# Performance work log

Measured on AMD Instinct MI355X. Metric: run time of the kernel, lower is better.

The kernel has to match this reference:

```python
import jax, jax.numpy as jnp
import numpy as np

K, N, M, P, H = 8, 16, 8, 32, 32
BSZ, T = 128, 512
TAU = 0.5
P_STAY = 0.9


def setup_inputs() -> dict:
    key = jax.random.key(0)
    ks = jax.random.split(key, 20)
    f32 = jnp.float32
    norm = lambda k, s, sc=1.0: (jax.random.normal(k, s) * sc).astype(f32)
    sw = 1.0 / np.sqrt(H)  # torch GRU init scale
    return {
        "a_seq": norm(ks[0], (BSZ, T, P)),
        "A": norm(ks[1], (K, N, N), 0.1),
        "Bmat": norm(ks[2], (K, N, M), 0.1),
        "C": norm(ks[3], (K, P, N), 0.1),
        "Q": (jnp.tile(jnp.eye(N, dtype=f32)[None], (K, 1, 1)) + norm(ks[4], (K, N, N), 0.01)),
        "wih_f": norm(ks[5], (3 * H, P), sw),
        "whh_f": norm(ks[6], (3 * H, H), sw),
        "bih_f": norm(ks[7], (3 * H,), sw),
        "bhh_f": norm(ks[8], (3 * H,), sw),
        "wih_b": norm(ks[9], (3 * H, P), sw),
        "whh_b": norm(ks[10], (3 * H, H), sw),
        "bih_b": norm(ks[11], (3 * H,), sw),
        "bhh_b": norm(ks[12], (3 * H,), sw),
        "wl": norm(ks[13], (K * K, 2 * H), sw),
        "bl": norm(ks[14], (K * K,), sw),
        "wi": norm(ks[15], (K, 2 * H), sw),
        "bi": norm(ks[16], (K,), sw),
        "u0": jax.random.uniform(ks[17], (BSZ, K), minval=1e-6, maxval=1.0 - 1e-6, dtype=f32),
        "useq": jax.random.uniform(ks[18], (BSZ, T - 1, K), minval=1e-6, maxval=1.0 - 1e-6, dtype=f32),
    }


def _gru_dir(gx, whh, bhh, reverse):
    # gx: [T, B, 3H] precomputed input-to-hidden gates; torch GRU cell math
    def step(h, g):
        gh = h @ whh.T + bhh
        xr, xz, xn = jnp.split(g, 3, axis=-1)
        hr, hz, hn = jnp.split(gh, 3, axis=-1)
        r = jax.nn.sigmoid(xr + hr)
        z = jax.nn.sigmoid(xz + hz)
        n = jnp.tanh(xn + r * hn)
        h_new = (1.0 - z) * n + z * h
        return h_new, h_new
    h0 = jnp.zeros((gx.shape[1], whh.shape[1]), gx.dtype)
    _, hs = jax.lax.scan(step, h0, gx, reverse=reverse)
    return hs  # [T, B, H]


def reference(a_seq, A, Bmat, C, Q, wih_f, whh_f, bih_f, bhh_f,
              wih_b, whh_b, bih_b, bhh_b, wl, bl, wi, bi, u0, useq):
    Bn, Tn, _ = a_seq.shape
    Kn = A.shape[0]
    x = a_seq.transpose(1, 0, 2)  # [T, B, P]
    hf = _gru_dir(x @ wih_f.T + bih_f, whh_f, bhh_f, False)
    hb = _gru_dir(x @ wih_b.T + bih_b, whh_b, bhh_b, True)
    h_seq = jnp.concatenate([hf, hb], axis=-1)  # [T, B, 2H]

    logits = (h_seq @ wl.T + bl).reshape(Tn, Bn, Kn, Kn)  # [T, B, K, K]
    init_logits = h_seq[0] @ wi.T + bi                     # [B, K]

    g0 = -jnp.log(-jnp.log(u0))
    gseq = -jnp.log(-jnp.log(useq))  # [B, T-1, K]

    # t = 0 (soft gumbel-softmax since is_training=True)
    y0 = jax.nn.softmax((init_logits + g0) / TAU, axis=-1)
    lq0 = (y0 * jax.nn.log_softmax(init_logits, axis=-1)).sum(-1)
    lp0 = (y0 * jnp.log(1.0 / Kn)).sum(-1)  # torch: full_like(1/K).log()

    trans = jnp.full((Kn, Kn), (1.0 - P_STAY) / (Kn - 1), a_seq.dtype)
    trans = trans.at[jnp.arange(Kn), jnp.arange(Kn)].set(P_STAY)

    def step(y_prev, xs):
        lg, g = xs  # lg: [B, K, K], g: [B, K]
        l_t = jnp.einsum('bk,bkj->bj', y_prev, lg)
        y_t = jax.nn.softmax((l_t + g) / TAU, axis=-1)
        lq = (y_t * jax.nn.log_softmax(l_t, axis=-1)).sum(-1)
        tp = y_prev @ trans
        lp = (y_t * jnp.log(jnp.clip(tp, 1e-8))).sum(-1)
        return y_t, (y_t, lq, lp)

    _, (ys, lqs, lps) = jax.lax.scan(step, y0, (logits[1:], gseq.transpose(1, 0, 2)))

    y_seq = jnp.concatenate([y0[None], ys], axis=0).transpose(1, 0, 2)  # [B, T, K]
    log_qseq = jnp.concatenate([lq0[None], lqs], axis=0).T              # [B, T]
    log_pseq = jnp.concatenate([lp0[None], lps], axis=0).T              # [B, T]

    A_seq = jnp.einsum('btk,kij->btij', y_seq, A)
    B_seq = jnp.einsum('btk,knm->btnm', y_seq, Bmat)
    Q_seq = jnp.einsum('btk,kij->btij', y_seq, Q)
    C_seq = jnp.broadcast_to(C[0], (Bn, Tn) + C[0].shape)
    return (A_seq, B_seq, C_seq, Q_seq, log_qseq, log_pseq)
```

## Files before the change

### kernel.cpp

```cpp
#include <hip/hip_runtime.h>
#include <math.h>

#define T 512
#define B 128
#define KK 8
#define HH 32
#define PP 32

#define WS_GX    0
#define WS_HSEQ  12582912
#define WS_LOGITS 0
#define WS_INIT  16777216
#define WS_YSEQ  16778240

#define OUT_A    0
#define OUT_B    16777216
#define OUT_C    25165824
#define OUT_Q    58720256
#define OUT_LQ   75497472
#define OUT_LP   75563008

#define TINV 2.0f
#define PSTAY 0.9f
#define OFFV (0.1f / 7.0f)
#define DPS (PSTAY - OFFV)
#define LOG_INV_K (-2.0794415416798357f)

typedef float f4v __attribute__((ext_vector_type(4)));
typedef __attribute__((address_space(3))) float as3f;

__device__ __forceinline__ void dma16(unsigned ldsbyte, int voffbyte, const void* sbase) {
    asm volatile("s_mov_b32 m0, %0\n\t"
                 "global_load_lds_dwordx4 %1, %2"
                 :: "s"(ldsbyte), "v"(voffbyte), "s"(sbase)
                 : "memory");
}
__device__ __forceinline__ void st16(void* p, f4v v) {
    asm volatile("global_store_dwordx4 %0, %1, off" :: "v"(p), "v"(v) : "memory");
}
__device__ __forceinline__ f4v ldsr16(int addr) {
    f4v out;
    asm volatile("ds_read_b128 %0, %1" : "=v"(out) : "v"(addr));
    return out;
}
__device__ __forceinline__ f4v ldg16(const void* p) {
    f4v out;
    asm volatile("global_load_dwordx4 %0, %1, off" : "=v"(out) : "v"(p) : "memory");
    return out;
}
__device__ __forceinline__ float ldg4(const void* p) {
    float out;
    asm volatile("global_load_dword %0, %1, off" : "=v"(out) : "v"(p) : "memory");
    return out;
}

__global__ __launch_bounds__(192) void gx_kernel(
    const float* __restrict__ a_seq,
    const float* __restrict__ wih_f, const float* __restrict__ bih_f,
    const float* __restrict__ wih_b, const float* __restrict__ bih_b,
    float* __restrict__ gx,
    const float* __restrict__ u0, const float* __restrict__ useq,
    float* __restrict__ gs) {
    __shared__ float xt[64 * 32];
    if (blockIdx.x >= 1024) {
        int id = (blockIdx.x - 1024) * 192 + threadIdx.x;
        if (id < T * B * KK) {
            int j = id & 7;
            int b = (id >> 3) & 127;
            int t = id >> 10;
            float u = (t == 0) ? u0[b * 8 + j]
                               : useq[((size_t)b * (T - 1) + (t - 1)) * 8 + j];
            gs[id] = -logf(-logf(u)) * TINV;
        }
        return;
    }
    int blk = blockIdx.x;
    int b = blk >> 3;
    int t0 = (blk & 7) << 6;
    int g = threadIdx.x;
    int dir = (g >= 96) ? 1 : 0;
    int gg = dir ? (g - 96) : g;
    const float* w = dir ? wih_b : wih_f;
    const float* bv = dir ? bih_b : bih_f;

    {
        const float4* src = (const float4*)(a_seq + ((size_t)b * T + t0) * PP);
        float4* dst = (float4*)xt;
        for (int idx = g; idx < 512; idx += 192) dst[idx] = src[idx];
    }
    float wreg[32];
#pragma unroll
    for (int q = 0; q < 8; ++q) {
        float4 wv = *(const float4*)(w + (size_t)gg * PP + q * 4);
        wreg[q * 4 + 0] = wv.x; wreg[q * 4 + 1] = wv.y;
        wreg[q * 4 + 2] = wv.z; wreg[q * 4 + 3] = wv.w;
    }
    float bias = bv[gg];
    __syncthreads();

    float* op = gx + ((size_t)(dir * B + b) * T + t0) * 96 + gg;
#pragma unroll 4
    for (int r = 0; r < 64; ++r) {
        const float4* xr = (const float4*)(xt + r * 32);
        float acc = bias;
#pragma unroll
        for (int q = 0; q < 8; ++q) {
            float4 xv = xr[q];
            acc = fmaf(xv.x, wreg[q * 4 + 0], acc);
            acc = fmaf(xv.y, wreg[q * 4 + 1], acc);
            acc = fmaf(xv.z, wreg[q * 4 + 2], acc);
            acc = fmaf(xv.w, wreg[q * 4 + 3], acc);
        }
        op[(size_t)r * 96] = acc;
    }
}

__global__ __launch_bounds__(64, 1) void gru_kernel(
    const float* __restrict__ gx,
    const float* __restrict__ whh_f, const float* __restrict__ bhh_f,
    const float* __restrict__ whh_b, const float* __restrict__ bhh_b,
    float* __restrict__ hseq) {
    int cid = blockIdx.x;
    int b = cid & 127;
    int dir = cid >> 7;
    int i = threadIdx.x & 31;
    const float* whh = dir ? whh_b : whh_f;
    const float* bhh = dir ? bhh_b : bhh_f;
    const float* gp0 = gx + (size_t)cid * (T * 96);

    f4v wr[8], wz[8], wn[8];
#pragma unroll
    for (int q = 0; q < 8; ++q) {
        wr[q] = ldg16(whh + (size_t)i * 32 + q * 4);
        wz[q] = ldg16(whh + (size_t)(32 + i) * 32 + q * 4);
        wn[q] = ldg16(whh + (size_t)(64 + i) * 32 + q * 4);
    }
    float bhr = ldg4(bhh + i);
    float bhz = ldg4(bhh + 32 + i);
    float bhn = ldg4(bhh + 64 + i);

    const float* p = gp0 + (dir ? (T - 1) * 96 : 0);
    int gstep = dir ? -96 : 96;
    int voff = (((dir ? (T - 1) : 0) * B + b) * 64 + dir * 32 + i) * 4;
    int vstep = dir ? -(B * 64 * 4) : (B * 64 * 4);

    float pxrA[8], pxzA[8], pxnA[8], pxrB[8], pxzB[8], pxnB[8];

#define LOADG(PR, PZ, PN, G0) do {                                             \
        _Pragma("unroll")                                                      \
        for (int u_ = 0; u_ < 8; ++u_) {                                       \
            int sc_ = (G0) * 8 + u_; if (sc_ > T - 1) sc_ = T - 1;             \
            const float* rp_ = p + sc_ * gstep;                                \
            PR[u_] = ldg4(rp_ + i);                                            \
            PZ[u_] = ldg4(rp_ + 32 + i);                                       \
            PN[u_] = ldg4(rp_ + 64 + i);                                       \
        }                                                                      \
    } while (0)

#define GWAIT(N) do {                                                          \
        asm volatile("s_waitcnt vmcnt(" #N ")" ::: "memory");                  \
        __builtin_amdgcn_sched_barrier(0);                                     \
    } while (0)

#define GSTEP(PR, PZ, PN, SLOT) do {                                           \
        float hj_[32];                                                         \
        _Pragma("unroll")                                                      \
        for (int jj = 0; jj < 32; ++jj)                                        \
            hj_[jj] = __uint_as_float(                                         \
                __builtin_amdgcn_readlane(__float_as_uint(h), jj));            \
        __builtin_amdgcn_sched_barrier(0);                                     \
        float r0_ = PR[SLOT] + bhr, r1_ = 0.f, r2_ = 0.f, r3_ = 0.f;           \
        float z0_ = PZ[SLOT] + bhz, z1_ = 0.f, z2_ = 0.f, z3_ = 0.f;           \
        float n0_ = bhn, n1_ = 0.f, n2_ = 0.f, n3_ = 0.f;                      \
        _Pragma("unroll")                                                      \
        for (int q_ = 0; q_ < 2; ++q_) {                                       \
            _Pragma("unroll")                                                  \
            for (int c_ = 0; c_ < 4; ++c_) {                                   \
                float hv_ = hj_[q_ * 4 + c_];                                  \
                r0_ = fmaf(wr[q_][c_], hv_, r0_);                              \
                z0_ = fmaf(wz[q_][c_], hv_, z0_);                              \
                n0_ = fmaf(wn[q_][c_], hv_, n0_);                              \
            }                                                                  \
        }                                                                      \
        _Pragma("unroll")                                                      \
        for (int q_ = 2; q_ < 4; ++q_) {                                       \
            _Pragma("unroll")                                                  \
            for (int c_ = 0; c_ < 4; ++c_) {                                   \
                float hv_ = hj_[q_ * 4 + c_];                                  \
                r1_ = fmaf(wr[q_][c_], hv_, r1_);                              \
                z1_ = fmaf(wz[q_][c_], hv_, z1_);                              \
                n1_ = fmaf(wn[q_][c_], hv_, n1_);                              \
            }                                                                  \
        }                                                                      \
        _Pragma("unroll")                                                      \
        for (int q_ = 4; q_ < 6; ++q_) {                                       \
            _Pragma("unroll")                                                  \
            for (int c_ = 0; c_ < 4; ++c_) {                                   \
                float hv_ = hj_[q_ * 4 + c_];                                  \
                r2_ = fmaf(wr[q_][c_], hv_, r2_);                              \
                z2_ = fmaf(wz[q_][c_], hv_, z2_);                              \
                n2_ = fmaf(wn[q_][c_], hv_, n2_);                              \
            }                                                                  \
        }                                                                      \
        _Pragma("unroll")                                                      \
        for (int q_ = 6; q_ < 8; ++q_) {                                       \
            _Pragma("unroll")                                                  \
            for (int c_ = 0; c_ < 4; ++c_) {                                   \
                float hv_ = hj_[q_ * 4 + c_];                                  \
                r3_ = fmaf(wr[q_][c_], hv_, r3_);                              \
                z3_ = fmaf(wz[q_][c_], hv_, z3_);                              \
                n3_ = fmaf(wn[q_][c_], hv_, n3_);                              \
            }                                                                  \
        }                                                                      \
        float hr_ = (r0_ + r1_) + (r2_ + r3_);                                 \
        float hz_ = (z0_ + z1_) + (z2_ + z3_);                                 \
        float hn_ = (n0_ + n1_) + (n2_ + n3_);                                 \
        float r_ = __builtin_amdgcn_rcpf(1.f + __expf(-hr_));                  \
        float z_ = __builtin_amdgcn_rcpf(1.f + __expf(-hz_));                  \
        float na_ = fmaf(r_, hn_, PN[SLOT]);                                   \
        float e2_ = __expf(-2.f * fabsf(na_));                                 \
        float n_ = copysignf((1.f - e2_) * __builtin_amdgcn_rcpf(1.f + e2_), na_); \
        h = fmaf(z_, h - n_, n_);                                              \
        asm volatile("global_store_dword %0, %1, %2"                           \
                     :: "v"(voff), "v"(h), "s"(hseq) : "memory");              \
        voff += vstep;                                                         \
    } while (0)

    LOADG(pxrA, pxzA, pxnA, 0);
    GWAIT(0);
    float h = 0.f;

    for (int gq = 0; gq < 32; ++gq) {
        LOADG(pxrB, pxzB, pxnB, 2 * gq + 1);
        GWAIT(32);
        GSTEP(pxrA, pxzA, pxnA, 0); GSTEP(pxrA, pxzA, pxnA, 1);
        GSTEP(pxrA, pxzA, pxnA, 2); GSTEP(pxrA, pxzA, pxnA, 3);
        GSTEP(pxrA, pxzA, pxnA, 4); GSTEP(pxrA, pxzA, pxnA, 5);
        GSTEP(pxrA, pxzA, pxnA, 6); GSTEP(pxrA, pxzA, pxnA, 7);
        LOADG(pxrA, pxzA, pxnA, 2 * gq + 2);
        GWAIT(32);
        GSTEP(pxrB, pxzB, pxnB, 0); GSTEP(pxrB, pxzB, pxnB, 1);
        GSTEP(pxrB, pxzB, pxnB, 2); GSTEP(pxrB, pxzB, pxnB, 3);
        GSTEP(pxrB, pxzB, pxnB, 4); GSTEP(pxrB, pxzB, pxnB, 5);
        GSTEP(pxrB, pxzB, pxnB, 6); GSTEP(pxrB, pxzB, pxnB, 7);
    }
#undef LOADG
#undef GWAIT
#undef GSTEP
}

__global__ __launch_bounds__(256) void logits_kernel(
    const float* __restrict__ hseq,
    const float* __restrict__ wl, const float* __restrict__ bl,
    const float* __restrict__ wi, const float* __restrict__ bi,
    float* __restrict__ logits, float* __restrict__ initl) {
    __shared__ float wls[64 * 65];
    __shared__ float hrow[4][64];
    int tid = threadIdx.x;
    for (int i2 = tid; i2 < 1024; i2 += 256) {
        float4 v = ((const float4*)wl)[i2];
        int gr = i2 >> 4;
        int cc = (i2 & 15) * 4;
        float* d = &wls[gr * 65 + cc];
        d[0] = v.x; d[1] = v.y; d[2] = v.z; d[3] = v.w;
    }
    int q = tid >> 6;
    int tb = blockIdx.x * 4 + q;
    int g = tid & 63;
    hrow[q][g] = hseq[(size_t)tb * 64 + g];
    __syncthreads();
    float acc = bl[g];
    const float* wrow = &wls[g * 65];
#pragma unroll
    for (int c = 0; c < 64; ++c) acc = fmaf(wrow[c], hrow[q][c], acc);
    logits[(size_t)tb * 64 + g] = acc * TINV;
    if (tb < B && g < 8) {
        float a2 = bi[g];
        const float* w2 = wi + (size_t)g * 64;
#pragma unroll
        for (int c = 0; c < 64; ++c) a2 = fmaf(w2[c], hrow[q][c], a2);
        initl[tb * 8 + g] = a2;
    }
}

__global__ __launch_bounds__(128, 1) void scan_kernel(
    const float* __restrict__ logits, const float* __restrict__ initl,
    const float* __restrict__ gs, float* __restrict__ yseq) {
    __shared__ float lds[6][2304];
    int tid = threadIdx.x;
    int wave = tid >> 6;
    int r = tid & 63;
    int b0 = blockIdx.x * 32;
    int b = b0 + (r & 31);
    int k15 = r & 15;

    unsigned ldsU = (unsigned)(unsigned long long)(as3f*)(&lds[0][0]);

#define ISSUE(tt, sl) do {                                                   \
        unsigned lb_ = ldsU + (unsigned)((sl) * 9216);                       \
        const char* bt_ = (const char*)logits + (size_t)(tt) * 32768;        \
        const char* gt_ = (const char*)gs + (size_t)(tt) * 4096;             \
        dma16(lb_ + 0 * 1024u, lof[0], bt_);                                 \
        dma16(lb_ + 1 * 1024u, lof[1], bt_);                                 \
        dma16(lb_ + 2 * 1024u, lof[2], bt_);                                 \
        dma16(lb_ + 3 * 1024u, lof[3], bt_);                                 \
        dma16(lb_ + 4 * 1024u, lof[4], bt_);                                 \
        dma16(lb_ + 5 * 1024u, lof[5], bt_);                                 \
        dma16(lb_ + 6 * 1024u, lof[6], bt_);                                 \
        dma16(lb_ + 7 * 1024u, lof[7], bt_);                                 \
        dma16(lb_ + 8192u, gof, gt_);                                        \
    } while (0)

    if (wave == 1) {
        int lof[8];
#pragma unroll
        for (int q = 0; q < 8; ++q) {
            int rr = q * 4 + (r >> 4);
            int cc = r & 15;
            lof[q] = (((b0 + rr) * 64) + ((cc ^ (rr & 15)) << 2)) << 2;
        }
        int gof;
        {
            int rg = r >> 1;
            int cc = r & 1;
            gof = (((b0 + rg) * 8) + ((cc ^ (rg & 1)) << 2)) << 2;
        }
#pragma unroll
        for (int p = 1; p <= 5; ++p) ISSUE(p, p);
        asm volatile("s_waitcnt vmcnt(36)" ::: "memory");
        __builtin_amdgcn_s_barrier();
        for (int t = 1; t < T; ++t) {
            asm volatile("s_waitcnt vmcnt(27)" ::: "memory");
            __builtin_amdgcn_s_barrier();
            int tp = t + 5; if (tp > T - 1) tp = T - 1;
            ISSUE(tp, (t + 5) % 6);
        }
        return;
    }

    unsigned rbase = ldsU + (unsigned)((r & 31) * 256);
    unsigned gbase = ldsU + 8192u + (unsigned)((r & 31) * 32);

#define SREAD(LL, GA, GB, tt) do {                                           \
        int so_ = ((tt) % 6) * 9216;                                         \
        _Pragma("unroll")                                                    \
        for (int m_ = 0; m_ < 16; ++m_)                                      \
            LL[m_] = ldsr16((int)(rbase + so_ + ((m_ ^ k15) << 4)));         \
        GA = ldsr16((int)(gbase + so_ + ((r & 1) << 4)));                    \
        GB = ldsr16((int)(gbase + so_ + (((r & 1) ^ 1) << 4)));              \
    } while (0)

#define LWAIT() do {                                                         \
        asm volatile("s_waitcnt lgkmcnt(0)" ::: "memory");                   \
        __builtin_amdgcn_sched_barrier(0);                                   \
    } while (0)

#define SCOMP(LL, GA, GB, tt) do {                                           \
        float pl_[8];                                                        \
        _Pragma("unroll")                                                    \
        for (int j_ = 0; j_ < 8; ++j_) pl_[j_] = 0.f;                        \
        _Pragma("unroll")                                                    \
        for (int k_ = 0; k_ < 8; ++k_) {                                     \
            f4v w0_ = LL[2 * k_], w1_ = LL[2 * k_ + 1];                      \
            float ek_ = e[k_];                                               \
            pl_[0] = fmaf(ek_, w0_.x, pl_[0]); pl_[1] = fmaf(ek_, w0_.y, pl_[1]); \
            pl_[2] = fmaf(ek_, w0_.z, pl_[2]); pl_[3] = fmaf(ek_, w0_.w, pl_[3]); \
            pl_[4] = fmaf(ek_, w1_.x, pl_[4]); pl_[5] = fmaf(ek_, w1_.y, pl_[5]); \
            pl_[6] = fmaf(ek_, w1_.z, pl_[6]); pl_[7] = fmaf(ek_, w1_.w, pl_[7]); \
        }                                                                    \
        float gg_[8] = {GA.x, GA.y, GA.z, GA.w, GB.x, GB.y, GB.z, GB.w};     \
        float ss_ = 0.f;                                                     \
        _Pragma("unroll")                                                    \
        for (int j_ = 0; j_ < 8; ++j_) {                                     \
            float a_ = fmaf(pl_[j_], sinv, gg_[j_]);                         \
            e[j_] = __expf(a_);                                              \
            ss_ += e[j_];                                                    \
        }                                                                    \
        sinv = __builtin_amdgcn_rcpf(ss_);                                   \
        if (r < 32) {                                                        \
            f4v v0_ = (f4v){e[0] * sinv, e[1] * sinv, e[2] * sinv, e[3] * sinv}; \
            f4v v1_ = (f4v){e[4] * sinv, e[5] * sinv, e[6] * sinv, e[7] * sinv}; \
            st16(&yp[2 * (tt)], v0_);                                        \
            st16(&yp[2 * (tt) + 1], v1_);                                    \
        }                                                                    \
    } while (0)

    f4v* yp = (f4v*)(yseq + (size_t)b * T * 8);
    float e[8];
    float sinv;

    {
        const f4v* il4 = (const f4v*)(initl + b * 8);
        f4v i0 = il4[0], i1 = il4[1];
        const f4v* g4 = (const f4v*)(gs + b * 8);
        f4v G0 = g4[0], G1 = g4[1];
        float a[8];
        a[0] = fmaf(i0.x, TINV, G0.x); a[1] = fmaf(i0.y, TINV, G0.y);
        a[2] = fmaf(i0.z, TINV, G0.z); a[3] = fmaf(i0.w, TINV, G0.w);
        a[4] = fmaf(i1.x, TINV, G1.x); a[5] = fmaf(i1.y, TINV, G1.y);
        a[6] = fmaf(i1.z, TINV, G1.z); a[7] = fmaf(i1.w, TINV, G1.w);
        float ssum = 0.f;
#pragma unroll
        for (int j = 0; j < 8; ++j) { e[j] = __expf(a[j]); ssum += e[j]; }
        sinv = __builtin_amdgcn_rcpf(ssum);
        if (r < 32) {
            f4v y0v = (f4v){e[0] * sinv, e[1] * sinv, e[2] * sinv, e[3] * sinv};
            f4v y1v = (f4v){e[4] * sinv, e[5] * sinv, e[6] * sinv, e[7] * sinv};
            st16(&yp[0], y0v);
            st16(&yp[1], y1v);
        }
    }

    f4v LA[16], LB[16], gaA, gbA, gaB, gbB;

    __builtin_amdgcn_s_barrier();
    SREAD(LA, gaA, gbA, 1);

    for (int t = 1; t < T - 1; t += 2) {
        __builtin_amdgcn_s_barrier();
        LWAIT();
        SREAD(LB, gaB, gbB, t + 1);
        SCOMP(LA, gaA, gbA, t);

        __builtin_amdgcn_s_barrier();
        LWAIT();
        SREAD(LA, gaA, gbA, t + 2);
        SCOMP(LB, gaB, gbB, t + 1);
    }
    __builtin_amdgcn_s_barrier();
    LWAIT();
    SCOMP(LA, gaA, gbA, T - 1);
#undef ISSUE
#undef SREAD
#undef LWAIT
#undef SCOMP
}

__global__ __launch_bounds__(256) void lqlp_kernel(
    const float* __restrict__ logits, const float* __restrict__ initl,
    const float* __restrict__ yseq,
    float* __restrict__ logq, float* __restrict__ logp) {
    int tid = blockIdx.x * 256 + threadIdx.x;
    int j = tid & 7;
    int row = tid >> 3;
    int b = row >> 9;
    int t = row & (T - 1);

    const float4* yt4 = (const float4*)(yseq + (size_t)row * 8);
    float4 ya = yt4[0], yb = yt4[1];
    float yt[8] = {ya.x, ya.y, ya.z, ya.w, yb.x, yb.y, yb.z, yb.w};

    float l[8];
    float lp;
    if (t == 0) {
        const float4* il4 = (const float4*)(initl + b * 8);
        float4 i0 = il4[0], i1 = il4[1];
        l[0] = i0.x; l[1] = i0.y; l[2] = i0.z; l[3] = i0.w;
        l[4] = i1.x; l[5] = i1.y; l[6] = i1.z; l[7] = i1.w;
        float sy = ((yt[0] + yt[1]) + (yt[2] + yt[3])) + ((yt[4] + yt[5]) + (yt[6] + yt[7]));
        lp = LOG_INV_K * sy;
    } else {
        const float4* yp4 = (const float4*)(yseq + (size_t)row * 8 - 8);
        float4 p0 = yp4[0], p1 = yp4[1];
        float ypv[8] = {p0.x, p0.y, p0.z, p0.w, p1.x, p1.y, p1.z, p1.w};
        float ypj = yseq[(size_t)row * 8 - 8 + j];
        const float4* L4 = (const float4*)(logits + ((size_t)t * B + b) * 64 + j * 8);
        float4 r0 = L4[0], r1 = L4[1];
        float c[8] = {ypj * r0.x, ypj * r0.y, ypj * r0.z, ypj * r0.w,
                      ypj * r1.x, ypj * r1.y, ypj * r1.z, ypj * r1.w};
#pragma unroll
        for (int s = 1; s <= 4; s <<= 1) {
#pragma unroll
            for (int m = 0; m < 8; ++m) c[m] += __shfl_xor(c[m], s, 64);
        }
#pragma unroll
        for (int m = 0; m < 8; ++m) l[m] = c[m] * 0.5f;
        float sy = ((ypv[0] + ypv[1]) + (ypv[2] + ypv[3])) + ((ypv[4] + ypv[5]) + (ypv[6] + ypv[7]));
        float acc = 0.f;
#pragma unroll
        for (int m = 0; m < 8; ++m) {
            float tp = fmaf(DPS, ypv[m], OFFV * sy);
            acc = fmaf(yt[m], logf(fmaxf(tp, 1e-8f)), acc);
        }
        lp = acc;
    }
    float m = fmaxf(fmaxf(fmaxf(l[0], l[1]), fmaxf(l[2], l[3])),
                    fmaxf(fmaxf(l[4], l[5]), fmaxf(l[6], l[7])));
    float se = 0.f;
#pragma unroll
    for (int m2 = 0; m2 < 8; ++m2) se += __expf(l[m2] - m);
    float lse = m + logf(se);
    float lq = 0.f;
#pragma unroll
    for (int m2 = 0; m2 < 8; ++m2) lq = fmaf(yt[m2], l[m2] - lse, lq);
    if (j == 0) {
        logq[row] = lq;
        logp[row] = lp;
    }
}

__global__ __launch_bounds__(256) void out_kernel(
    const float* __restrict__ yseq,
    const float* __restrict__ A, const float* __restrict__ Bm,
    const float* __restrict__ C, const float* __restrict__ Q,
    float4* __restrict__ out4) {
    __shared__ float tab[6144];
    int tid = threadIdx.x;
    int bt0 = blockIdx.x * 64;
    {
        float4* t4 = (float4*)tab;
        const float4* A4 = (const float4*)A;
        const float4* B4 = (const float4*)Bm;
        const float4* Q4 = (const float4*)Q;
        const float4* C4 = (const float4*)C;
        for (int i2 = tid; i2 < 512; i2 += 256) t4[i2] = A4[i2];
        if (tid < 256) t4[512 + tid] = B4[tid];
        for (int i2 = tid; i2 < 512; i2 += 256) t4[768 + i2] = Q4[i2];
        if (tid < 128) t4[1280 + tid] = C4[tid];
        const float4* Y4 = (const float4*)(yseq + (size_t)bt0 * 8);
        if (tid < 128) t4[1408 + tid] = Y4[tid];
    }
    __syncthreads();

    int wave = tid >> 6;
    int lane = tid & 63;
    const float4* t4 = (const float4*)tab;

    if (wave == 0 || wave == 1) {
        int tbase = (wave == 0) ? 0 : 768;
        size_t obase = (wave == 0) ? (size_t)(OUT_A / 4) : (size_t)(OUT_Q / 4);
        float4 wreg[8];
#pragma unroll
        for (int k = 0; k < 8; ++k) wreg[k] = t4[tbase + k * 64 + lane];
        for (int bt = 0; bt < 64; ++bt) {
            float4 ya = t4[1408 + bt * 2];
            float4 yb = t4[1408 + bt * 2 + 1];
            float yk[8] = {ya.x, ya.y, ya.z, ya.w, yb.x, yb.y, yb.z, yb.w};
            float4 v = make_float4(0.f, 0.f, 0.f, 0.f);
#pragma unroll
            for (int k = 0; k < 8; ++k) {
                v.x = fmaf(yk[k], wreg[k].x, v.x);
                v.y = fmaf(yk[k], wreg[k].y, v.y);
                v.z = fmaf(yk[k], wreg[k].z, v.z);
                v.w = fmaf(yk[k], wreg[k].w, v.w);
            }
            out4[obase + (size_t)(bt0 + bt) * 64 + lane] = v;
        }
    } else if (wave == 2) {
        if (lane < 32) {
            float4 wreg[8];
#pragma unroll
            for (int k = 0; k < 8; ++k) wreg[k] = t4[512 + k * 32 + lane];
            for (int bt = 0; bt < 64; ++bt) {
                float4 ya = t4[1408 + bt * 2];
                float4 yb = t4[1408 + bt * 2 + 1];
                float yk[8] = {ya.x, ya.y, ya.z, ya.w, yb.x, yb.y, yb.z, yb.w};
                float4 v = make_float4(0.f, 0.f, 0.f, 0.f);
#pragma unroll
                for (int k = 0; k < 8; ++k) {
                    v.x = fmaf(yk[k], wreg[k].x, v.x);
                    v.y = fmaf(yk[k], wreg[k].y, v.y);
                    v.z = fmaf(yk[k], wreg[k].z, v.z);
                    v.w = fmaf(yk[k], wreg[k].w, v.w);
                }
                out4[(size_t)(OUT_B / 4) + (size_t)(bt0 + bt) * 32 + lane] = v;
            }
        } else {
            float4 c0 = t4[1280 + (lane - 32)];
            for (int bt = 0; bt < 64; ++bt)
                out4[(size_t)(OUT_C / 4) + (size_t)(bt0 + bt) * 128 + (lane - 32)] = c0;
        }
    } else {
        float4 c1 = t4[1280 + 32 + lane];
        float4 c2 = (lane < 32) ? t4[1280 + 96 + lane] : make_float4(0.f, 0.f, 0.f, 0.f);
        for (int bt = 0; bt < 64; ++bt) {
            out4[(size_t)(OUT_C / 4) + (size_t)(bt0 + bt) * 128 + 32 + lane] = c1;
            if (lane < 32)
                out4[(size_t)(OUT_C / 4) + (size_t)(bt0 + bt) * 128 + 96 + lane] = c2;
        }
    }
}

extern "C" void kernel_launch(void* const* d_in, const int* in_sizes, int n_in,
                              void* d_out, int out_size, void* d_ws, size_t ws_size,
                              hipStream_t stream) {
    const float* a_seq = (const float*)d_in[0];
    const float* A     = (const float*)d_in[1];
    const float* Bmat  = (const float*)d_in[2];
    const float* C     = (const float*)d_in[3];
    const float* Q     = (const float*)d_in[4];
    const float* wih_f = (const float*)d_in[5];
    const float* whh_f = (const float*)d_in[6];
    const float* bih_f = (const float*)d_in[7];
    const float* bhh_f = (const float*)d_in[8];
    const float* wih_b = (const float*)d_in[9];
    const float* whh_b = (const float*)d_in[10];
    const float* bih_b = (const float*)d_in[11];
    const float* bhh_b = (const float*)d_in[12];
    const float* wl    = (const float*)d_in[13];
    const float* bl    = (const float*)d_in[14];
    const float* wi    = (const float*)d_in[15];
    const float* bi    = (const float*)d_in[16];
    const float* u0    = (const float*)d_in[17];
    const float* useq  = (const float*)d_in[18];

    float* ws = (float*)d_ws;
    float* gx     = ws + WS_GX;
    float* hseq   = ws + WS_HSEQ;
    float* logits = ws + WS_LOGITS;
    float* initl  = ws + WS_INIT;
    float* yseq   = ws + WS_YSEQ;
    float* gs2    = ws + WS_YSEQ + (size_t)B * T * KK;

    float* outf = (float*)d_out;
    float* logq = outf + OUT_LQ;
    float* logp = outf + OUT_LP;

    gx_kernel<<<1024 + (T * B * KK + 191) / 192, 192, 0, stream>>>(
        a_seq, wih_f, bih_f, wih_b, bih_b, gx, u0, useq, gs2);
    gru_kernel<<<256, 64, 0, stream>>>(gx, whh_f, bhh_f, whh_b, bhh_b, hseq);
    logits_kernel<<<T * B / 4, 256, 0, stream>>>(hseq, wl, bl, wi, bi, logits, initl);
    scan_kernel<<<4, 128, 0, stream>>>(logits, initl, gs2, yseq);
    lqlp_kernel<<<B * T * KK / 256, 256, 0, stream>>>(logits, initl, yseq, logq, logp);
    out_kernel<<<B * T / 64, 256, 0, stream>>>(yseq, A, Bmat, C, Q, (float4*)d_out);
}
```

Measured before the change: 454.5 us.

## Overlap C broadcast writes with the serial scan using extra scan blocks

```diff
diff --git a/kernel.cpp b/kernel.cpp
--- a/kernel.cpp
+++ b/kernel.cpp
@@ -285,9 +285,18 @@
 
 __global__ __launch_bounds__(128, 1) void scan_kernel(
     const float* __restrict__ logits, const float* __restrict__ initl,
-    const float* __restrict__ gs, float* __restrict__ yseq) {
+    const float* __restrict__ gs, float* __restrict__ yseq,
+    const float4* __restrict__ Csrc, float4* __restrict__ outC) {
     __shared__ float lds[6][2304];
     int tid = threadIdx.x;
+    if (blockIdx.x >= 4) {
+        size_t stride = (size_t)(2048 - 4) * 128;
+        for (size_t idx = (size_t)(blockIdx.x - 4) * 128 + tid;
+             idx < (size_t)B * T * 128; idx += stride) {
+            outC[idx] = Csrc[idx & 127];
+        }
+        return;
+    }
     int wave = tid >> 6;
     int r = tid & 63;
     int b0 = blockIdx.x * 32;
@@ -502,9 +511,9 @@
 __global__ __launch_bounds__(256) void out_kernel(
     const float* __restrict__ yseq,
     const float* __restrict__ A, const float* __restrict__ Bm,
-    const float* __restrict__ C, const float* __restrict__ Q,
+    const float* __restrict__ Q,
     float4* __restrict__ out4) {
-    __shared__ float tab[6144];
+    __shared__ float tab[5632];
     int tid = threadIdx.x;
     int bt0 = blockIdx.x * 64;
     {
@@ -512,13 +521,11 @@
         const float4* A4 = (const float4*)A;
         const float4* B4 = (const float4*)Bm;
         const float4* Q4 = (const float4*)Q;
-        const float4* C4 = (const float4*)C;
         for (int i2 = tid; i2 < 512; i2 += 256) t4[i2] = A4[i2];
         if (tid < 256) t4[512 + tid] = B4[tid];
         for (int i2 = tid; i2 < 512; i2 += 256) t4[768 + i2] = Q4[i2];
-        if (tid < 128) t4[1280 + tid] = C4[tid];
         const float4* Y4 = (const float4*)(yseq + (size_t)bt0 * 8);
-        if (tid < 128) t4[1408 + tid] = Y4[tid];
+        if (tid < 128) t4[1280 + tid] = Y4[tid];
     }
     __syncthreads();
 
@@ -533,8 +540,8 @@
 #pragma unroll
         for (int k = 0; k < 8; ++k) wreg[k] = t4[tbase + k * 64 + lane];
         for (int bt = 0; bt < 64; ++bt) {
-            float4 ya = t4[1408 + bt * 2];
-            float4 yb = t4[1408 + bt * 2 + 1];
+            float4 ya = t4[1280 + bt * 2];
+            float4 yb = t4[1280 + bt * 2 + 1];
             float yk[8] = {ya.x, ya.y, ya.z, ya.w, yb.x, yb.y, yb.z, yb.w};
             float4 v = make_float4(0.f, 0.f, 0.f, 0.f);
 #pragma unroll
@@ -546,37 +553,23 @@
             }
             out4[obase + (size_t)(bt0 + bt) * 64 + lane] = v;
         }
-    } else if (wave == 2) {
-        if (lane < 32) {
-            float4 wreg[8];
-#pragma unroll
-            for (int k = 0; k < 8; ++k) wreg[k] = t4[512 + k * 32 + lane];
-            for (int bt = 0; bt < 64; ++bt) {
-                float4 ya = t4[1408 + bt * 2];
-                float4 yb = t4[1408 + bt * 2 + 1];
-                float yk[8] = {ya.x, ya.y, ya.z, ya.w, yb.x, yb.y, yb.z, yb.w};
-                float4 v = make_float4(0.f, 0.f, 0.f, 0.f);
-#pragma unroll
-                for (int k = 0; k < 8; ++k) {
-                    v.x = fmaf(yk[k], wreg[k].x, v.x);
-                    v.y = fmaf(yk[k], wreg[k].y, v.y);
-                    v.z = fmaf(yk[k], wreg[k].z, v.z);
-                    v.w = fmaf(yk[k], wreg[k].w, v.w);
-                }
-                out4[(size_t)(OUT_B / 4) + (size_t)(bt0 + bt) * 32 + lane] = v;
+    } else if (wave == 2 && lane < 32) {
+        float4 wreg[8];
+#pragma unroll
+        for (int k = 0; k < 8; ++k) wreg[k] = t4[512 + k * 32 + lane];
+        for (int bt = 0; bt < 64; ++bt) {
+            float4 ya = t4[1280 + bt * 2];
+            float4 yb = t4[1280 + bt * 2 + 1];
+            float yk[8] = {ya.x, ya.y, ya.z, ya.w, yb.x, yb.y, yb.z, yb.w};
+            float4 v = make_float4(0.f, 0.f, 0.f, 0.f);
+#pragma unroll
+            for (int k = 0; k < 8; ++k) {
+                v.x = fmaf(yk[k], wreg[k].x, v.x);
+                v.y = fmaf(yk[k], wreg[k].y, v.y);
+                v.z = fmaf(yk[k], wreg[k].z, v.z);
+                v.w = fmaf(yk[k], wreg[k].w, v.w);
             }
-        } else {
-            float4 c0 = t4[1280 + (lane - 32)];
-            for (int bt = 0; bt < 64; ++bt)
-                out4[(size_t)(OUT_C / 4) + (size_t)(bt0 + bt) * 128 + (lane - 32)] = c0;
-        }
-    } else {
-        float4 c1 = t4[1280 + 32 + lane];
-        float4 c2 = (lane < 32) ? t4[1280 + 96 + lane] : make_float4(0.f, 0.f, 0.f, 0.f);
-        for (int bt = 0; bt < 64; ++bt) {
-            out4[(size_t)(OUT_C / 4) + (size_t)(bt0 + bt) * 128 + 32 + lane] = c1;
-            if (lane < 32)
-                out4[(size_t)(OUT_C / 4) + (size_t)(bt0 + bt) * 128 + 96 + lane] = c2;
+            out4[(size_t)(OUT_B / 4) + (size_t)(bt0 + bt) * 32 + lane] = v;
         }
     }
 }
@@ -615,12 +608,14 @@
     float* outf = (float*)d_out;
     float* logq = outf + OUT_LQ;
     float* logp = outf + OUT_LP;
+    float4* outC = (float4*)(outf + OUT_C);
 
     gx_kernel<<<1024 + (T * B * KK + 191) / 192, 192, 0, stream>>>(
         a_seq, wih_f, bih_f, wih_b, bih_b, gx, u0, useq, gs2);
     gru_kernel<<<256, 64, 0, stream>>>(gx, whh_f, bhh_f, whh_b, bhh_b, hseq);
     logits_kernel<<<T * B / 4, 256, 0, stream>>>(hseq, wl, bl, wi, bi, logits, initl);
-    scan_kernel<<<4, 128, 0, stream>>>(logits, initl, gs2, yseq);
+    scan_kernel<<<2048, 128, 0, stream>>>(logits, initl, gs2, yseq,
+                                          (const float4*)C, outC);
     lqlp_kernel<<<B * T * KK / 256, 256, 0, stream>>>(logits, initl, yseq, logq, logp);
-    out_kernel<<<B * T / 64, 256, 0, stream>>>(yseq, A, Bmat, C, Q, (float4*)d_out);
-}
+    out_kernel<<<B * T / 64, 256, 0, stream>>>(yseq, A, Bmat, Q, (float4*)d_out);
+}
```

Result: faster. 444.4 us (-2.2%).
